# Optimization experiments

Measured on AMD Instinct MI355X. Metric: run time of the kernel, lower is better.

Reference implementation:

```python
import jax, jax.numpy as jnp
import numpy as np

B, N, COUT, CIN, H, W = 16, 4, 256, 256, 64, 64


def setup_inputs() -> dict:
    key = jax.random.key(0)
    k1, k2, k3, k4 = jax.random.split(key, 4)
    x = jax.random.normal(k1, (B, CIN, H, W), jnp.float32)
    alphas = jax.random.uniform(k2, (B, N), jnp.float32)          # routing weights (lambdas)
    angles = jax.random.normal(k3, (B, N), jnp.float32) * 0.5     # thetas, mixed signs
    # kaiming_normal_(mode='fan_out', relu): std = sqrt(2 / (Cout * k * k))
    std = np.sqrt(2.0 / (COUT * 9)).astype(np.float32)
    weight = jax.random.normal(k4, (N, COUT, CIN, 3, 3), jnp.float32) * std
    return {"x": x, "alphas": alphas, "angles": angles, "weight": weight}


def _rot_mats(thetas):
    """thetas: [M] -> rotation matrices [M, 9, 9] (row, col), matching torch builder."""
    xc = jnp.cos(thetas)
    ys = jnp.sin(thetas)
    a = xc - ys
    b = xc * ys
    c = xc + ys
    z = jnp.zeros_like(xc)
    o = jnp.ones_like(xc)

    def mat(rows):
        # rows: list of 9 lists of 9 [M]-arrays -> [M, 9, 9]
        return jnp.stack([jnp.stack(r, axis=-1) for r in rows], axis=-2)

    pos = mat([
        [a, 1 - a, z, z, z, z, z, z, z],
        [z, xc - b, b, z, 1 - c + b, ys - b, z, z, z],
        [z, z, a, z, z, 1 - a, z, z, z],
        [b, ys - b, z, xc - b, 1 - c + b, z, z, z, z],
        [z, z, z, z, o, z, z, z, z],
        [z, z, z, z, 1 - c + b, xc - b, z, ys - b, b],
        [z, z, z, 1 - a, z, z, a, z, z],
        [z, z, z, ys - b, 1 - c + b, z, b, xc - b, z],
        [z, z, z, z, z, z, z, 1 - a, a],
    ])
    neg = mat([
        [c, z, z, 1 - c, z, z, z, z, z],
        [-b, xc + b, z, b - ys, 1 - a - b, z, z, z, z],
        [z, 1 - c, c, z, z, z, z, z, z],
        [z, z, z, xc + b, 1 - a - b, z, -b, b - ys, z],
        [z, z, z, z, o, z, z, z, z],
        [z, b - ys, -b, z, 1 - a - b, xc + b, z, z, z],
        [z, z, z, z, z, z, c, 1 - c, z],
        [z, z, z, z, 1 - a - b, b - ys, z, xc + b, -b],
        [z, z, z, z, z, 1 - c, z, z, c],
    ])
    m = (thetas >= 0).astype(thetas.dtype)[:, None, None]
    return m * pos + (1 - m) * neg


def reference(x, alphas, angles, weight):
    bsz, Cin, h, w = x.shape
    n, Cout = weight.shape[0], weight.shape[1]
    # [bsz, n, 9, 9] rotation matrices scaled by routing lambdas
    rm = _rot_mats(angles.reshape(-1)).reshape(bsz, n, 9, 9)
    rm = rm * alphas[:, :, None, None]
    # weights [n, Cout, Cin, 3, 3] -> [n, 9, Cout*Cin]
    Wf = weight.transpose(0, 3, 4, 1, 2).reshape(n, 9, Cout * Cin)
    # mix over kernel_number n and source tap q -> per-sample rotated kernels
    rw = jnp.einsum('bnpq,nqm->bpm', rm, Wf)          # [bsz, 9, Cout*Cin]
    rw = rw.reshape(bsz, 3, 3, Cout, Cin).transpose(0, 3, 4, 1, 2)
    rw = rw.reshape(bsz * Cout, Cin, 3, 3)
    # per-sample conv via grouped conv on flattened batch
    xr = x.reshape(1, bsz * Cin, h, w)
    out = jax.lax.conv_general_dilated(
        xr, rw, window_strides=(1, 1), padding=((1, 1), (1, 1)),
        dimension_numbers=('NCHW', 'OIHW', 'NCHW'), feature_group_count=bsz)
    return out.reshape(bsz, Cout, out.shape[2], out.shape[3])
```

## Files before the change

### kernel.cpp

```cpp
#include <hip/hip_runtime.h>
#include <hip/hip_bf16.h>

#define B_    16
#define N_    4
#define COUT  256
#define CIN   256
#define H_    64
#define W_    64
#define K_TOT (CIN * 9)
#define HW    (H_ * W_)
#define NKT   (K_TOT / 64)
#define PAD   66
#define PLANE (PAD * PAD)

typedef __attribute__((ext_vector_type(8))) short short8;
typedef __attribute__((ext_vector_type(4))) float f32x4;
typedef unsigned short ushort_t;

static __device__ __forceinline__ ushort_t f2bf(float f) {
    __hip_bfloat16 h = __float2bfloat16(f);
    return *reinterpret_cast<ushort_t*>(&h);
}

typedef __attribute__((address_space(3))) unsigned int lds_u32;
typedef __attribute__((address_space(1))) const unsigned int glb_u32;
static __device__ __forceinline__ void gl_lds16(const ushort_t* g, ushort_t* l) {
    __builtin_amdgcn_global_load_lds((glb_u32*)g, (lds_u32*)l, 16, 0, 0);
}

#define BARRIER() asm volatile("s_barrier" ::: "memory")
#define VMCNT0()  asm volatile("s_waitcnt vmcnt(0)" ::: "memory")

__global__ void rot_mats_kernel(const float* __restrict__ alphas,
                                const float* __restrict__ angles,
                                float* __restrict__ rm) {
    int i = threadIdx.x;
    if (i >= B_ * N_) return;
    float th = angles[i], al = alphas[i];
    float xc = cosf(th), ys = sinf(th);
    float a = xc - ys, b = xc * ys, c = xc + ys;
    float r[81];
#pragma unroll
    for (int j = 0; j < 81; ++j) r[j] = 0.f;
    if (th >= 0.f) {
        r[0] = a;          r[1] = 1.f - a;
        r[10] = xc - b;    r[11] = b;        r[13] = 1.f - c + b; r[14] = ys - b;
        r[20] = a;         r[23] = 1.f - a;
        r[27] = b;         r[28] = ys - b;   r[30] = xc - b;      r[31] = 1.f - c + b;
        r[40] = 1.f;
        r[49] = 1.f - c + b; r[50] = xc - b; r[52] = ys - b;      r[53] = b;
        r[57] = 1.f - a;   r[60] = a;
        r[66] = ys - b;    r[67] = 1.f - c + b; r[69] = b;        r[70] = xc - b;
        r[79] = 1.f - a;   r[80] = a;
    } else {
        r[0] = c;          r[3] = 1.f - c;
        r[9] = -b;         r[10] = xc + b;   r[12] = b - ys;      r[13] = 1.f - a - b;
        r[19] = 1.f - c;   r[20] = c;
        r[30] = xc + b;    r[31] = 1.f - a - b; r[33] = -b;       r[34] = b - ys;
        r[40] = 1.f;
        r[46] = b - ys;    r[47] = -b;       r[49] = 1.f - a - b; r[50] = xc + b;
        r[60] = c;         r[61] = 1.f - c;
        r[67] = 1.f - a - b; r[68] = b - ys; r[70] = xc + b;      r[71] = -b;
        r[77] = 1.f - c;   r[80] = c;
    }
#pragma unroll
    for (int j = 0; j < 81; ++j) rm[i * 81 + j] = r[j] * al;
}

__global__ __launch_bounds__(256)
void build_rw_kernel(const float* __restrict__ weight,
                     const float* __restrict__ rm,
                     ushort_t* __restrict__ rw) {
    __shared__ float rms[N_ * 81];
    int tid = threadIdx.x;
    int b = blockIdx.y;
    for (int j = tid; j < N_ * 81; j += 256)
        rms[j] = rm[b * N_ * 81 + j];
    __syncthreads();

    int idx = blockIdx.x * 256 + tid;
    int cout = idx >> 8, cin = idx & 255;

    float wv[N_][9];
#pragma unroll
    for (int n = 0; n < N_; ++n)
#pragma unroll
        for (int q = 0; q < 9; ++q)
            wv[n][q] = weight[(size_t)(n * (COUT * CIN) + idx) * 9 + q];

    ushort_t* dst = rw + (size_t)(b * COUT + cout) * K_TOT + cin;
#pragma unroll
    for (int p = 0; p < 9; ++p) {
        float s = 0.f;
#pragma unroll
        for (int n = 0; n < N_; ++n)
#pragma unroll
            for (int q = 0; q < 9; ++q)
                s += rms[n * 81 + p * 9 + q] * wv[n][q];
        dst[p * 256] = f2bf(s);
    }
}

__global__ __launch_bounds__(256)
void halo_zero_kernel(ushort_t* __restrict__ xt) {
    ushort_t* base = xt + (size_t)blockIdx.x * PLANE * 64;
    int t = threadIdx.x;
    for (int i = t; i < 260; i += 256) {
        int py, px;
        if (i < 66)       { py = 0;  px = i; }
        else if (i < 132) { py = 65; px = i - 66; }
        else if (i < 196) { py = i - 132 + 1; px = 0; }
        else              { py = i - 196 + 1; px = 65; }
        ushort_t* d = base + (size_t)(py * PAD + px) * 64;
        int4 z = {0, 0, 0, 0};
#pragma unroll
        for (int q = 0; q < 8; ++q) *(int4*)(d + q * 8) = z;
    }
}

__global__ __launch_bounds__(256)
void nhwc_kernel(const float* __restrict__ x, ushort_t* __restrict__ xt) {
    int y    = blockIdx.x;
    int cb32 = blockIdx.y;
    int b    = blockIdx.z;
    __shared__ ushort_t tileT[64][40];
    int t = threadIdx.x;

    int ci = t & 31, seg = t >> 5;
    const float* src = x + ((size_t)(b * CIN + cb32 * 32 + ci) * HW + y * 64 + seg * 8);
    float4 f0 = ((const float4*)src)[0];
    float4 f1 = ((const float4*)src)[1];
#pragma unroll
    for (int q = 0; q < 4; ++q) tileT[seg * 8 + q][ci]     = f2bf(((float*)&f0)[q]);
#pragma unroll
    for (int q = 0; q < 4; ++q) tileT[seg * 8 + 4 + q][ci] = f2bf(((float*)&f1)[q]);
    __syncthreads();

    int px = t >> 2, cseg = t & 3;
    ushort_t* dst = xt + ((size_t)(b * 4 + (cb32 >> 1)) * PLANE + (y + 1) * PAD + px + 1) * 64
                       + (cb32 & 1) * 32 + cseg * 8;
    *(int4*)dst = *(const int4*)&tileT[px][cseg * 8];
}

__global__ __launch_bounds__(512, 1)
void conv_kernel(const ushort_t* __restrict__ xt,
                 const ushort_t* __restrict__ rw,
                 float* __restrict__ out) {
    int bid0 = blockIdx.x;
    int bid = (bid0 & 7) * 32 + (bid0 >> 3);
    int b    = bid >> 4;
    int tile = bid & 15;
    int y0 = tile * 4;
    int tid = threadIdx.x;
    int lane = tid & 63, wid = tid >> 6;
    int wm = wid >> 2, wn = wid & 3;
    int rA = lane & 15, kseg = lane >> 4;

    __shared__ __align__(16) ushort_t As[2][256][64];
    __shared__ __align__(16) ushort_t Bs[2][256][64];
    ushort_t* AsB = &As[0][0][0];
    ushort_t* BsB = &Bs[0][0][0];

    f32x4 acc[8][4] = {};

    const ushort_t* rwb = rw + (size_t)b * COUT * K_TOT;
    const ushort_t* xtb = xt + (size_t)b * 4 * PLANE * 64;

    const int sd = (lane & 7) ^ (lane >> 3);
    const int r0 = wid * 16 + (lane >> 3);
    const int a00 = (r0      ) * K_TOT + sd * 8;
    const int a01 = (r0 +   8) * K_TOT + sd * 8;
    const int a10 = (r0 + 128) * K_TOT + sd * 8;
    const int a11 = (r0 + 136) * K_TOT + sd * 8;
    const int d00 = (2 * wid + 0) * 512 + lane * 8;
    const int d01 = (2 * wid + 1) * 512 + lane * 8;
    const int d10 = 8192 + d00;
    const int d11 = 8192 + d01;
    int p00, p01, p10, p11;
    {
        int pr, prow, pcol;
        pr = r0;         prow = pr >> 6; pcol = pr & 63; p00 = (prow * PAD + pcol) * 64 + sd * 8;
        pr = r0 + 8;     prow = pr >> 6; pcol = pr & 63; p01 = (prow * PAD + pcol) * 64 + sd * 8;
        pr = r0 + 128;   prow = pr >> 6; pcol = pr & 63; p10 = (prow * PAD + pcol) * 64 + sd * 8;
        pr = r0 + 136;   prow = pr >> 6; pcol = pr & 63; p11 = (prow * PAD + pcol) * 64 + sd * 8;
    }

#define STAGE_A(KTN, QN)                                                       \
    {                                                                          \
        int p_ = (KTN) >> 2, c4_ = (KTN) & 3;                                  \
        int ako = p_ * 256 + c4_ * 64;                                         \
        ushort_t* db = AsB + (QN) * 16384;                                     \
        gl_lds16(rwb + a00 + ako, db + d00);                                   \
        gl_lds16(rwb + a01 + ako, db + d01);                                   \
        gl_lds16(rwb + a10 + ako, db + d10);                                   \
        gl_lds16(rwb + a11 + ako, db + d11);                                   \
    }

#define STAGE_B(KTN, QN)                                                       \
    {                                                                          \
        int p_ = (KTN) >> 2, c4_ = (KTN) & 3;                                  \
        int ph_ = p_ / 3, pw_ = p_ - 3 * ph_;                                  \
        const ushort_t* sb = xtb + (size_t)(c4_ * PLANE + (y0 + ph_) * PAD + pw_) * 64; \
        ushort_t* db = BsB + (QN) * 16384;                                     \
        gl_lds16(sb + p00, db + d00);                                          \
        gl_lds16(sb + p01, db + d01);                                          \
        gl_lds16(sb + p10, db + d10);                                          \
        gl_lds16(sb + p11, db + d11);                                          \
    }

#define READ_AF(Q, MH2, KH)                                                    \
    _Pragma("unroll")                                                          \
    for (int mi = 0; mi < 4; ++mi) {                                           \
        int row = wm * 128 + (MH2) * 64 + mi * 16 + rA;                        \
        af[mi] = *(const short8*)(AsB + (Q) * 16384 + row * 64                 \
                                  + ((((KH) << 2) | kseg) ^ (rA & 7)) * 8);    \
    }

#define READ_BF(Q, KH)                                                         \
    _Pragma("unroll")                                                          \
    for (int ni = 0; ni < 4; ++ni) {                                           \
        int row = wn * 64 + ni * 16 + rA;                                      \
        bf[ni] = *(const short8*)(BsB + (Q) * 16384 + row * 64                 \
                                  + ((((KH) << 2) | kseg) ^ (rA & 7)) * 8);    \
    }

#define DO_MFMA(MH2)                                                           \
    __builtin_amdgcn_s_setprio(1);                                             \
    _Pragma("unroll")                                                          \
    for (int mi = 0; mi < 4; ++mi)                                             \
        _Pragma("unroll")                                                      \
        for (int ni = 0; ni < 4; ++ni)                                         \
            acc[(MH2) * 4 + mi][ni] = __builtin_amdgcn_mfma_f32_16x16x32_bf16( \
                af[mi], bf[ni], acc[(MH2) * 4 + mi][ni], 0, 0, 0);             \
    __builtin_amdgcn_s_setprio(0);

    STAGE_A(0, 0);
    STAGE_B(0, 0);
    VMCNT0();
    BARRIER();

    short8 af[4], bf[4];
    for (int kt = 0; kt < NKT; ++kt) {
        int q = kt & 1, qn = q ^ 1;
        bool more = (kt + 1 < NKT);
        READ_AF(q, 0, 0);
        READ_BF(q, 0);
        if (more) STAGE_A(kt + 1, qn);
        BARRIER();
        DO_MFMA(0);
        BARRIER();
        READ_AF(q, 1, 0);
        if (more) STAGE_B(kt + 1, qn);
        BARRIER();
        DO_MFMA(1);
        BARRIER();
        READ_AF(q, 0, 1);
        READ_BF(q, 1);
        BARRIER();
        DO_MFMA(0);
        BARRIER();
        READ_AF(q, 1, 1);
        BARRIER();
        DO_MFMA(1);
        VMCNT0();
        BARRIER();
    }
#undef STAGE_A
#undef STAGE_B
#undef READ_AF
#undef READ_BF
#undef DO_MFMA

    int row0 = (lane >> 4) * 4;
    int col  = lane & 15;
    float* outb = out + (size_t)b * COUT * HW + tile * 256;
#pragma unroll
    for (int am = 0; am < 8; ++am)
#pragma unroll
        for (int an = 0; an < 4; ++an)
#pragma unroll
            for (int rr = 0; rr < 4; ++rr) {
                int m = wm * 128 + am * 16 + row0 + rr;
                int n = wn * 64 + an * 16 + col;
                outb[(size_t)m * HW + n] = acc[am][an][rr];
            }
}

extern "C" void kernel_launch(void* const* d_in, const int* in_sizes, int n_in,
                              void* d_out, int out_size, void* d_ws, size_t ws_size,
                              hipStream_t stream) {
    const float* x      = (const float*)d_in[0];
    const float* alphas = (const float*)d_in[1];
    const float* angles = (const float*)d_in[2];
    const float* weight = (const float*)d_in[3];
    float* out = (float*)d_out;

    ushort_t* rw = (ushort_t*)d_ws;
    ushort_t* xt = (ushort_t*)((char*)d_ws + (size_t)B_ * COUT * K_TOT * 2);
    float*    rm = (float*)((char*)d_ws + (size_t)B_ * COUT * K_TOT * 2
                                        + (size_t)64 * PLANE * 64 * 2);

    rot_mats_kernel<<<1, 64, 0, stream>>>(alphas, angles, rm);
    build_rw_kernel<<<dim3(COUT * CIN / 256, B_), 256, 0, stream>>>(weight, rm, rw);
    halo_zero_kernel<<<64, 256, 0, stream>>>(xt);
    nhwc_kernel<<<dim3(64, 8, B_), 256, 0, stream>>>(x, xt);
    conv_kernel<<<256, 512, 0, stream>>>(xt, rw, out);
}
```

Baseline: 117.1 us.

## Switch conv GEMM to 4-stage pipeline with 32-wide K tiles

The conv GEMM main loop moves from a double-buffered 64-wide K tile to a four-slot ring of 32-wide K tiles, issuing loads three iterations ahead and waiting with partial vmcnt counts instead of draining all loads each iteration. The LDS layout and XOR swizzle are redone for 32-element rows, and load indexing is recomputed per thread. The aim is to hide global-load latency behind more in-flight stages and to cut full vmcnt(0) stalls. In exchange there are twice as many iterations, so barrier overhead per MFMA rises, and the hand-tuned vmcnt counts must match the exact number of outstanding loads.

```diff
diff --git a/kernel.cpp b/kernel.cpp
--- a/kernel.cpp
+++ b/kernel.cpp
@@ -9,7 +9,7 @@
 #define W_    64
 #define K_TOT (CIN * 9)
 #define HW    (H_ * W_)
-#define NKT   (K_TOT / 64)
+#define NKT   (K_TOT / 32)
 #define PAD   66
 #define PLANE (PAD * PAD)
 
@@ -29,7 +29,7 @@
 }
 
 #define BARRIER() asm volatile("s_barrier" ::: "memory")
-#define VMCNT0()  asm volatile("s_waitcnt vmcnt(0)" ::: "memory")
+#define VMCNTN(N) asm volatile("s_waitcnt vmcnt(" #N ")" ::: "memory")
 
 __global__ void rot_mats_kernel(const float* __restrict__ alphas,
                                 const float* __restrict__ angles,
@@ -156,72 +156,61 @@
     int wm = wid >> 2, wn = wid & 3;
     int rA = lane & 15, kseg = lane >> 4;
 
-    __shared__ __align__(16) ushort_t As[2][256][64];
-    __shared__ __align__(16) ushort_t Bs[2][256][64];
+    __shared__ __align__(16) ushort_t As[4][256][32];
+    __shared__ __align__(16) ushort_t Bs[4][256][32];
     ushort_t* AsB = &As[0][0][0];
     ushort_t* BsB = &Bs[0][0][0];
 
     f32x4 acc[8][4] = {};
 
-    const ushort_t* rwb = rw + (size_t)b * COUT * K_TOT;
-    const ushort_t* xtb = xt + (size_t)b * 4 * PLANE * 64;
-
-    const int sd = (lane & 7) ^ (lane >> 3);
-    const int r0 = wid * 16 + (lane >> 3);
-    const int a00 = (r0      ) * K_TOT + sd * 8;
-    const int a01 = (r0 +   8) * K_TOT + sd * 8;
-    const int a10 = (r0 + 128) * K_TOT + sd * 8;
-    const int a11 = (r0 + 136) * K_TOT + sd * 8;
-    const int d00 = (2 * wid + 0) * 512 + lane * 8;
-    const int d01 = (2 * wid + 1) * 512 + lane * 8;
-    const int d10 = 8192 + d00;
-    const int d11 = 8192 + d01;
-    int p00, p01, p10, p11;
-    {
-        int pr, prow, pcol;
-        pr = r0;         prow = pr >> 6; pcol = pr & 63; p00 = (prow * PAD + pcol) * 64 + sd * 8;
-        pr = r0 + 8;     prow = pr >> 6; pcol = pr & 63; p01 = (prow * PAD + pcol) * 64 + sd * 8;
-        pr = r0 + 128;   prow = pr >> 6; pcol = pr & 63; p10 = (prow * PAD + pcol) * 64 + sd * 8;
-        pr = r0 + 136;   prow = pr >> 6; pcol = pr & 63; p11 = (prow * PAD + pcol) * 64 + sd * 8;
-    }
-
-#define STAGE_A(KTN, QN)                                                       \
+    const ushort_t* rwb  = rw + (size_t)b * COUT * K_TOT;
+    const ushort_t* xtb2 = xt + (size_t)b * 4 * PLANE * 64 + (size_t)y0 * PAD * 64;
+
+    const int r0 = tid >> 2;
+    const int sd = tid & 3;
+    const int fs = (r0 & 3) ^ ((r0 >> 2) & 3);
+    const int sg = (sd ^ fs) * 8;
+    const int a0 = r0 * K_TOT + sg;
+    const int a1 = (r0 + 128) * K_TOT + sg;
+    const int pb0 = ((r0 >> 6) * PAD + (r0 & 63)) * 64 + sg;
+    const int pb1 = pb0 + 2 * PAD * 64;
+    const int dd0 = tid * 8;
+    const int dd1 = 4096 + tid * 8;
+    const int fread = (rA & 3) ^ ((rA >> 2) & 3);
+    const int cread = (kseg ^ fread) * 8;
+
+#define STAGE_A(KTN)                                                           \
     {                                                                          \
-        int p_ = (KTN) >> 2, c4_ = (KTN) & 3;                                  \
-        int ako = p_ * 256 + c4_ * 64;                                         \
-        ushort_t* db = AsB + (QN) * 16384;                                     \
-        gl_lds16(rwb + a00 + ako, db + d00);                                   \
-        gl_lds16(rwb + a01 + ako, db + d01);                                   \
-        gl_lds16(rwb + a10 + ako, db + d10);                                   \
-        gl_lds16(rwb + a11 + ako, db + d11);                                   \
-    }
-
-#define STAGE_B(KTN, QN)                                                       \
+        int p_ = (KTN) >> 3, c32_ = (KTN) & 7;                                 \
+        int ako = p_ * 256 + c32_ * 32;                                        \
+        ushort_t* db = AsB + ((KTN) & 3) * 8192;                               \
+        gl_lds16(rwb + a0 + ako, db + dd0);                                    \
+        gl_lds16(rwb + a1 + ako, db + dd1);                                    \
+    }
+
+#define STAGE_B(KTN)                                                           \
     {                                                                          \
-        int p_ = (KTN) >> 2, c4_ = (KTN) & 3;                                  \
+        int p_ = (KTN) >> 3, cb4_ = ((KTN) & 7) >> 1, h_ = (KTN) & 1;          \
         int ph_ = p_ / 3, pw_ = p_ - 3 * ph_;                                  \
-        const ushort_t* sb = xtb + (size_t)(c4_ * PLANE + (y0 + ph_) * PAD + pw_) * 64; \
-        ushort_t* db = BsB + (QN) * 16384;                                     \
-        gl_lds16(sb + p00, db + d00);                                          \
-        gl_lds16(sb + p01, db + d01);                                          \
-        gl_lds16(sb + p10, db + d10);                                          \
-        gl_lds16(sb + p11, db + d11);                                          \
-    }
-
-#define READ_AF(Q, MH2, KH)                                                    \
+        const ushort_t* sb = xtb2 + (size_t)(cb4_ * PLANE + ph_ * PAD + pw_) * 64 \
+                             + h_ * 32;                                        \
+        ushort_t* db = BsB + ((KTN) & 3) * 8192;                               \
+        gl_lds16(sb + pb0, db + dd0);                                          \
+        gl_lds16(sb + pb1, db + dd1);                                          \
+    }
+
+#define READ_AF(Q, MH2)                                                        \
     _Pragma("unroll")                                                          \
     for (int mi = 0; mi < 4; ++mi) {                                           \
         int row = wm * 128 + (MH2) * 64 + mi * 16 + rA;                        \
-        af[mi] = *(const short8*)(AsB + (Q) * 16384 + row * 64                 \
-                                  + ((((KH) << 2) | kseg) ^ (rA & 7)) * 8);    \
-    }
-
-#define READ_BF(Q, KH)                                                         \
+        af[mi] = *(const short8*)(AsB + (Q) * 8192 + row * 32 + cread);        \
+    }
+
+#define READ_BF(Q)                                                             \
     _Pragma("unroll")                                                          \
     for (int ni = 0; ni < 4; ++ni) {                                           \
         int row = wn * 64 + ni * 16 + rA;                                      \
-        bf[ni] = *(const short8*)(BsB + (Q) * 16384 + row * 64                 \
-                                  + ((((KH) << 2) | kseg) ^ (rA & 7)) * 8);    \
+        bf[ni] = *(const short8*)(BsB + (Q) * 8192 + row * 32 + cread);        \
     }
 
 #define DO_MFMA(MH2)                                                           \
@@ -234,35 +223,29 @@
                 af[mi], bf[ni], acc[(MH2) * 4 + mi][ni], 0, 0, 0);             \
     __builtin_amdgcn_s_setprio(0);
 
-    STAGE_A(0, 0);
-    STAGE_B(0, 0);
-    VMCNT0();
+    STAGE_A(0); STAGE_B(0);
+    STAGE_A(1); STAGE_B(1);
+    STAGE_A(2); STAGE_B(2);
+    VMCNTN(8);
     BARRIER();
 
     short8 af[4], bf[4];
     for (int kt = 0; kt < NKT; ++kt) {
-        int q = kt & 1, qn = q ^ 1;
-        bool more = (kt + 1 < NKT);
-        READ_AF(q, 0, 0);
-        READ_BF(q, 0);
-        if (more) STAGE_A(kt + 1, qn);
+        int q = kt & 3;
+        bool more = (kt + 3 < NKT);
+        READ_AF(q, 0);
+        READ_BF(q);
+        if (more) STAGE_A(kt + 3);
         BARRIER();
         DO_MFMA(0);
         BARRIER();
-        READ_AF(q, 1, 0);
-        if (more) STAGE_B(kt + 1, qn);
+        READ_AF(q, 1);
+        if (more) STAGE_B(kt + 3);
         BARRIER();
         DO_MFMA(1);
-        BARRIER();
-        READ_AF(q, 0, 1);
-        READ_BF(q, 1);
-        BARRIER();
-        DO_MFMA(0);
-        BARRIER();
-        READ_AF(q, 1, 1);
-        BARRIER();
-        DO_MFMA(1);
-        VMCNT0();
+        if (kt < NKT - 3)       { VMCNTN(8); }
+        else if (kt == NKT - 3) { VMCNTN(4); }
+        else if (kt == NKT - 2) { VMCNTN(0); }
         BARRIER();
     }
 #undef STAGE_A
```

Result: slower. 124.6 us (+6.4%).
